# Kernel tuning notes

Hardware: AMD Instinct MI355X
Metric: run time of the kernel (lower is better)

The kernel has to match this reference:

```python
import jax, jax.numpy as jnp
import numpy as np

BEAM = 64  # min(beam_size=64, num_states=512)


def setup_inputs() -> dict:
    key = jax.random.key(0)
    ks = jax.random.split(key, 8)
    B, N, S, E, F, D = 8, 1024, 512, 2048, 256, 32
    unaries = jax.random.normal(ks[0], (B, N, S), jnp.float32)
    masks = jnp.ones((B, N), dtype=bool)
    binary_edges = jax.random.randint(ks[1], (B, E, 2), 0, N)
    binary_masks = jnp.ones((B, E), dtype=bool)
    node_features = jax.random.normal(ks[2], (B, N, F), jnp.float32)
    targets = jax.random.randint(ks[3], (B, N), 0, S)
    # learned params
    bin_embed = jax.random.uniform(ks[4], (2, S, D), jnp.float32)  # torch.rand init
    W_dyn = jax.random.normal(ks[5], (2 * F, D * D), jnp.float32) / jnp.sqrt(2.0 * F)
    b_dyn = jnp.zeros((D * D,), jnp.float32)
    return dict(unaries=unaries, masks=masks, binary_edges=binary_edges,
                binary_masks=binary_masks, node_features=node_features,
                targets=targets, bin_embed=bin_embed, W_dyn=W_dyn, b_dyn=b_dyn)


def reference(unaries, masks, binary_edges, binary_masks, node_features,
              targets, bin_embed, W_dyn, b_dyn):
    B, N, S = unaries.shape
    D = bin_embed.shape[-1]
    mf = masks.astype(unaries.dtype)
    un = unaries * mf[..., None]  # mask unaries

    # put target state first in the beam (scatter +inf, then topk indices)
    big = jnp.asarray(1e30, un.dtype)
    _un = jax.lax.stop_gradient(un).at[
        jnp.arange(B)[:, None], jnp.arange(N)[None, :], targets].set(big)
    _, beam_targets = jax.lax.top_k(_un, BEAM)               # [B,N,K] int
    beam_unary = jnp.take_along_axis(un, beam_targets, axis=2)  # [B,N,K]

    # gather beam state-ids and node features at edge endpoints
    e0, e1 = binary_edges[..., 0], binary_edges[..., 1]      # [B,E]
    bt0 = jnp.take_along_axis(beam_targets, e0[:, :, None], axis=1)  # [B,E,K]
    bt1 = jnp.take_along_axis(beam_targets, e1[:, :, None], axis=1)
    s0 = bin_embed[0][bt0]                                   # [B,E,K,D]
    s1 = bin_embed[1][bt1]                                   # [B,E,K,D]
    f0 = jnp.take_along_axis(node_features, e0[:, :, None], axis=1)  # [B,E,F]
    f1 = jnp.take_along_axis(node_features, e1[:, :, None], axis=1)
    feat = jnp.concatenate([f0, f1], axis=-1)                # [B,E,2F]
    ew = jax.nn.relu(feat @ W_dyn + b_dyn)                   # [B,E,D*D]
    ew = ew.reshape(B, -1, D, D)                             # [B,E,D,D]

    # low-rank binary potentials: B E K1 D1, B E D1 D2, B E K2 D2 -> B E K1 K2
    bin_phis = jnp.einsum('beki,beij,belj->bekl', s0, ew, s1)

    # piecewise pseudo-likelihood
    norm_unary = jax.nn.log_softmax(beam_unary, axis=-1)
    gold_unary = jnp.where(masks, norm_unary[:, :, 0], 0.0)
    pll = gold_unary.sum(-1)                                 # [B]

    E = bin_phis.shape[1]
    norm_bin = jax.nn.log_softmax(bin_phis.reshape(B, E, BEAM * BEAM), axis=-1)
    gold_bin = jnp.where(binary_masks, norm_bin[:, :, 0], 0.0)  # index (0,0)
    pll = pll + gold_bin.sum(-1)

    nll = -(pll / mf.sum(-1)).mean()
    return nll
```

## Files before the change

### kernel.cpp

```cpp
#include <hip/hip_runtime.h>
#include <hip/hip_bf16.h>
#include <math.h>

#define BATCH  8
#define NNODE  1024
#define NSTATE 512
#define NEDGE  2048
#define NFEAT  256
#define DDIM   32
#define KBEAM  64

typedef __attribute__((ext_vector_type(8))) short bf16x8;
typedef __attribute__((ext_vector_type(4))) float f32x4;
typedef unsigned short u16;
typedef unsigned long long u64;

__device__ __forceinline__ u16 f2b(float f) {
  __hip_bfloat16 h = __float2bfloat16(f);
  return *reinterpret_cast<u16*>(&h);
}

__global__ __launch_bounds__(256) void beam_kernel(
    const float* __restrict__ unaries,
    const int*   __restrict__ targets,
    int*         __restrict__ beam_ids,
    float*       __restrict__ ugold)
{
  const int tid  = threadIdx.x;
  const int lane = tid & 63, wid = tid >> 6;
  const int node = blockIdx.x * 4 + wid;
  const float* row = unaries + (size_t)node * NSTATE;
  const int target = targets[node];

  float v[8];
  float4 va = *(const float4*)(row + lane * 4);
  float4 vb = *(const float4*)(row + 256 + lane * 4);
  v[0]=va.x; v[1]=va.y; v[2]=va.z; v[3]=va.w;
  v[4]=vb.x; v[5]=vb.y; v[6]=vb.z; v[7]=vb.w;

  u64 key[8]; int idx[8];
  #pragma unroll
  for (int t = 0; t < 8; t++) {
    int i = (t < 4) ? lane * 4 + t : 256 + lane * 4 + (t - 4);
    idx[t] = i;
    unsigned u = __float_as_uint(v[t]);
    unsigned k = (u & 0x80000000u) ? ~u : (u | 0x80000000u);
    if (i == target) k = 0xFFFFFFFFu;
    key[t] = ((u64)k << 9) | (unsigned)(NSTATE - 1 - i);
  }

  unsigned act = 0xFFu;
  int K = KBEAM;
  for (int b = 40; b >= 0; b--) {
    unsigned m1 = 0;
    #pragma unroll
    for (int t = 0; t < 8; t++)
      m1 |= ((unsigned)((key[t] >> b) & 1ull)) << t;
    int c = __popc(m1 & act);
    #pragma unroll
    for (int off = 32; off > 0; off >>= 1) c += __shfl_xor(c, off);
    if (c >= K) act &= m1; else { K -= c; act = act & ~m1; }
  }
  u64 thr = 0;
  #pragma unroll
  for (int t = 0; t < 8; t++) if (act & (1u << t)) thr = key[t];
  {
    unsigned lo = (unsigned)thr, hi = (unsigned)(thr >> 32);
    #pragma unroll
    for (int off = 32; off > 0; off >>= 1) {
      lo |= __shfl_xor(lo, off); hi |= __shfl_xor(hi, off);
    }
    thr = ((u64)hi << 32) | lo;
  }

  unsigned sel = 0;
  #pragma unroll
  for (int t = 0; t < 8; t++) if (key[t] >= thr) sel |= 1u << t;

  float m = v[0];
  #pragma unroll
  for (int t = 1; t < 8; t++) m = fmaxf(m, v[t]);
  #pragma unroll
  for (int off = 32; off > 0; off >>= 1) m = fmaxf(m, __shfl_xor(m, off));
  float s = 0.0f, tv = 0.0f;
  #pragma unroll
  for (int t = 0; t < 8; t++) {
    if (sel & (1u << t)) s += __expf(v[t] - m);
    if (idx[t] == target) tv = v[t];
  }
  #pragma unroll
  for (int off = 32; off > 0; off >>= 1) {
    s += __shfl_xor(s, off); tv += __shfl_xor(tv, off);
  }
  if (lane == 0) ugold[node] = tv - (m + __logf(s));

  int* bout = beam_ids + (size_t)node * KBEAM;
  unsigned selnt = sel;
  #pragma unroll
  for (int t = 0; t < 8; t++)
    if (idx[t] == target) { selnt &= ~(1u << t); bout[0] = target; }
  int base = 1;
  #pragma unroll
  for (int t = 0; t < 8; t++) {
    u64 bt = __ballot((selnt >> t) & 1u);
    if ((selnt >> t) & 1u) {
      int pos = base + __popcll(bt & ((1ull << lane) - 1ull));
      bout[pos] = idx[t];
    }
    base += __popcll(bt);
  }
}

__global__ __launch_bounds__(256) void conv_embed_kernel(
    const float* __restrict__ in, u16* __restrict__ out) {
  int idx = (blockIdx.x * 256 + threadIdx.x) * 4;
  float4 v = *(const float4*)(in + idx);
  ushort4 o; o.x = f2b(v.x); o.y = f2b(v.y); o.z = f2b(v.z); o.w = f2b(v.w);
  *(ushort4*)(out + idx) = o;
}

__global__ __launch_bounds__(256) void convW_kernel(
    const float* __restrict__ W, u16* __restrict__ Wt) {
  __shared__ u16 tile[64][64];
  const int tid = threadIdx.x;
  const int n0 = blockIdx.x * 64;
  const int k0 = blockIdx.y * 64;
  #pragma unroll
  for (int p = 0; p < 4; p++) {
    int k  = (tid >> 4) + p * 16;
    int nc = (tid & 15) * 4;
    float4 v = *(const float4*)(W + (size_t)(k0 + k) * 1024 + n0 + nc);
    tile[nc + 0][k] = f2b(v.x); tile[nc + 1][k] = f2b(v.y);
    tile[nc + 2][k] = f2b(v.z); tile[nc + 3][k] = f2b(v.w);
  }
  __syncthreads();
  int n = tid >> 2, kc = (tid & 3) * 16;
  uint4 o0 = *(uint4*)&tile[n][kc];
  uint4 o1 = *(uint4*)&tile[n][kc + 8];
  *(uint4*)(Wt + (size_t)(n0 + n) * 512 + k0 + kc)     = o0;
  *(uint4*)(Wt + (size_t)(n0 + n) * 512 + k0 + kc + 8) = o1;
}

__global__ __launch_bounds__(128) void gatherA_kernel(
    const float* __restrict__ nf, const int* __restrict__ edges,
    u16* __restrict__ A) {
  const int eg = blockIdx.x;
  const int t  = threadIdx.x;
  const int b  = eg >> 11;
  const int n0 = edges[eg * 2 + 0], n1 = edges[eg * 2 + 1];
  const float* src = (t < 64)
      ? nf + ((size_t)(b * NNODE + n0) * NFEAT) + t * 4
      : nf + ((size_t)(b * NNODE + n1) * NFEAT) + (t - 64) * 4;
  float4 v = *(const float4*)src;
  ushort4 o; o.x = f2b(v.x); o.y = f2b(v.y); o.z = f2b(v.z); o.w = f2b(v.w);
  *(ushort4*)(A + (size_t)eg * 512 + t * 4) = o;
}

__global__ __launch_bounds__(256) void gemm_mfma_kernel(
    const u16* __restrict__ A,
    const u16* __restrict__ Bt,
    const float* __restrict__ bias,
    u16* __restrict__ ew)
{
  __shared__ u16 As[128 * 32];
  __shared__ u16 Bs[128 * 32];
  const int tid  = threadIdx.x;
  const int lane = tid & 63, wid = tid >> 6;
  const int wr = wid >> 1, wc = wid & 1;
  const int fr = lane & 15, fg = lane >> 4;
  const int row0 = blockIdx.y * 128, col0 = blockIdx.x * 128;

  const int sr = tid >> 2, sc = (tid & 3) * 8;
  const u16* aptr  = A  + (size_t)(row0 + sr) * 512 + sc;
  const u16* bptr  = Bt + (size_t)(col0 + sr) * 512 + sc;
  const u16* aptr2 = aptr + (size_t)64 * 512;
  const u16* bptr2 = bptr + (size_t)64 * 512;

  f32x4 acc[4][4] = {};
  uint4 ra  = *(const uint4*)aptr,  ra2 = *(const uint4*)aptr2;
  uint4 rb  = *(const uint4*)bptr,  rb2 = *(const uint4*)bptr2;

  for (int ks = 0; ks < 16; ks++) {
    __syncthreads();
    *(uint4*)&As[sr * 32 + sc]        = ra;
    *(uint4*)&As[(sr + 64) * 32 + sc] = ra2;
    *(uint4*)&Bs[sr * 32 + sc]        = rb;
    *(uint4*)&Bs[(sr + 64) * 32 + sc] = rb2;
    __syncthreads();
    if (ks < 15) {
      int ko = (ks + 1) * 32;
      ra  = *(const uint4*)(aptr  + ko); ra2 = *(const uint4*)(aptr2 + ko);
      rb  = *(const uint4*)(bptr  + ko); rb2 = *(const uint4*)(bptr2 + ko);
    }
    bf16x8 af[4], bfr[4];
    #pragma unroll
    for (int mb = 0; mb < 4; mb++)
      af[mb] = *(bf16x8*)&As[(wr * 64 + mb * 16 + fr) * 32 + fg * 8];
    #pragma unroll
    for (int nb = 0; nb < 4; nb++)
      bfr[nb] = *(bf16x8*)&Bs[(wc * 64 + nb * 16 + fr) * 32 + fg * 8];
    #pragma unroll
    for (int mb = 0; mb < 4; mb++)
      #pragma unroll
      for (int nb = 0; nb < 4; nb++)
        acc[mb][nb] = __builtin_amdgcn_mfma_f32_16x16x32_bf16(
            af[mb], bfr[nb], acc[mb][nb], 0, 0, 0);
  }

  #pragma unroll
  for (int nb = 0; nb < 4; nb++) {
    int col = col0 + wc * 64 + nb * 16 + fr;
    float bc = bias[col];
    #pragma unroll
    for (int mb = 0; mb < 4; mb++) {
      #pragma unroll
      for (int r = 0; r < 4; r++) {
        int rowm = row0 + wr * 64 + mb * 16 + fg * 4 + r;
        float v = fmaxf(acc[mb][nb][r] + bc, 0.0f);
        ew[(size_t)rowm * 1024 + col] = f2b(v);
      }
    }
  }
}

#define EW_LDS 5120
__global__ __launch_bounds__(256) void edge_mfma_kernel(
    const u16* __restrict__ embed,
    const int* __restrict__ edges,
    const u16* __restrict__ ewb,
    const int* __restrict__ beam_ids,
    float*     __restrict__ egold)
{
  __shared__ u16 esh[4 * EW_LDS];
  const int tid  = threadIdx.x;
  const int lane = tid & 63, wid = tid >> 6;
  u16* s0  = &esh[wid * EW_LDS];
  u16* s1u = s0 + 2048;
  u16* ewl = s0 + 4096;

  const int eg = blockIdx.x * 4 + wid;
  const int b  = eg >> 11;
  const int n0 = edges[eg * 2 + 0], n1 = edges[eg * 2 + 1];
  const int bt0 = beam_ids[(size_t)(b * NNODE + n0) * KBEAM + lane];
  const int bt1 = beam_ids[(size_t)(b * NNODE + n1) * KBEAM + lane];

  #pragma unroll
  for (int s = 0; s < 4; s++) {
    int r = s * 16 + (lane >> 2);
    int e0 = __shfl(bt0, r), e1 = __shfl(bt1, r);
    uint4 v0 = *(const uint4*)(embed + (size_t)e0 * DDIM + (lane & 3) * 8);
    uint4 v1 = *(const uint4*)(embed + (size_t)NSTATE * DDIM
                               + (size_t)e1 * DDIM + (lane & 3) * 8);
    *(uint4*)&s0 [r * 32 + (lane & 3) * 8] = v0;
    *(uint4*)&s1u[r * 32 + (lane & 3) * 8] = v1;
  }
  #pragma unroll
  for (int s = 0; s < 2; s++) {
    uint4 v = *(const uint4*)(ewb + (size_t)eg * 1024 + s * 512 + lane * 8);
    *(uint4*)&ewl[s * 512 + lane * 8] = v;
  }
  asm volatile("s_waitcnt lgkmcnt(0)" ::: "memory");

  const int fr = lane & 15, fg = lane >> 4;
  bf16x8 a1[4], bew[2];
  #pragma unroll
  for (int mb = 0; mb < 4; mb++)
    a1[mb] = *(bf16x8*)&s1u[(mb * 16 + fr) * 32 + fg * 8];
  #pragma unroll
  for (int nb = 0; nb < 2; nb++)
    bew[nb] = *(bf16x8*)&ewl[(nb * 16 + fr) * 32 + fg * 8];
  f32x4 uacc[4][2] = {};
  #pragma unroll
  for (int mb = 0; mb < 4; mb++)
    #pragma unroll
    for (int nb = 0; nb < 2; nb++)
      uacc[mb][nb] = __builtin_amdgcn_mfma_f32_16x16x32_bf16(
          a1[mb], bew[nb], uacc[mb][nb], 0, 0, 0);

  asm volatile("s_waitcnt lgkmcnt(0)" ::: "memory");
  #pragma unroll
  for (int mb = 0; mb < 4; mb++)
    #pragma unroll
    for (int nb = 0; nb < 2; nb++)
      #pragma unroll
      for (int r = 0; r < 4; r++) {
        int l = mb * 16 + fg * 4 + r;
        int i = nb * 16 + fr;
        s1u[l * 32 + i] = f2b(uacc[mb][nb][r]);
      }
  asm volatile("s_waitcnt lgkmcnt(0)" ::: "memory");

  bf16x8 a0[4], bu[4];
  #pragma unroll
  for (int mb = 0; mb < 4; mb++)
    a0[mb] = *(bf16x8*)&s0[(mb * 16 + fr) * 32 + fg * 8];
  #pragma unroll
  for (int nb = 0; nb < 4; nb++)
    bu[nb] = *(bf16x8*)&s1u[(nb * 16 + fr) * 32 + fg * 8];
  f32x4 facc[4][4] = {};
  #pragma unroll
  for (int mb = 0; mb < 4; mb++)
    #pragma unroll
    for (int nb = 0; nb < 4; nb++)
      facc[mb][nb] = __builtin_amdgcn_mfma_f32_16x16x32_bf16(
          a0[mb], bu[nb], facc[mb][nb], 0, 0, 0);

  float mx = -INFINITY;
  #pragma unroll
  for (int mb = 0; mb < 4; mb++)
    #pragma unroll
    for (int nb = 0; nb < 4; nb++)
      #pragma unroll
      for (int r = 0; r < 4; r++) mx = fmaxf(mx, facc[mb][nb][r]);
  #pragma unroll
  for (int off = 32; off > 0; off >>= 1) mx = fmaxf(mx, __shfl_xor(mx, off));
  float s = 0.0f;
  #pragma unroll
  for (int mb = 0; mb < 4; mb++)
    #pragma unroll
    for (int nb = 0; nb < 4; nb++)
      #pragma unroll
      for (int r = 0; r < 4; r++) s += __expf(facc[mb][nb][r] - mx);
  #pragma unroll
  for (int off = 32; off > 0; off >>= 1) s += __shfl_xor(s, off);
  if (lane == 0) {
    egold[eg] = facc[0][0][0] - mx - __logf(s);
  }
}

__global__ __launch_bounds__(1024) void reduce_kernel(
    const float* __restrict__ ugold,
    const float* __restrict__ egold,
    float* __restrict__ out) {
  __shared__ float red[16];
  const int tid = threadIdx.x;
  float s = 0.0f;
  #pragma unroll
  for (int t = 0; t < 8; t++)  s += ugold[tid + t * 1024];
  #pragma unroll
  for (int t = 0; t < 16; t++) s += egold[tid + t * 1024];
  #pragma unroll
  for (int off = 32; off > 0; off >>= 1) s += __shfl_xor(s, off);
  if ((tid & 63) == 0) red[tid >> 6] = s;
  __syncthreads();
  if (tid == 0) {
    float tot = 0.0f;
    #pragma unroll
    for (int w = 0; w < 16; w++) tot += red[w];
    out[0] = -tot / (float)(BATCH * NNODE);
  }
}

extern "C" void kernel_launch(void* const* d_in, const int* in_sizes, int n_in,
                              void* d_out, int out_size, void* d_ws, size_t ws_size,
                              hipStream_t stream) {
  (void)in_sizes; (void)n_in; (void)out_size; (void)ws_size;
  const float* unaries   = (const float*)d_in[0];
  const int*   edges     = (const int*)  d_in[2];
  const float* nf        = (const float*)d_in[4];
  const int*   targets   = (const int*)  d_in[5];
  const float* bin_embed = (const float*)d_in[6];
  const float* W         = (const float*)d_in[7];
  const float* bias      = (const float*)d_in[8];
  float* out = (float*)d_out;

  char* ws = (char*)d_ws;
  float* ugold = (float*)ws;
  float* egold = (float*)(ws + (32u<<10));
  int*  beam_ids = (int*)(ws + (1u<<20));
  u16*  Abf = (u16*)(ws + (3u<<20));
  u16*  Wt  = (u16*)(ws + (19u<<20));
  u16*  ewb = (u16*)(ws + (20u<<20));
  u16*  emb = (u16*)(ws + (52u<<20));

  beam_kernel<<<BATCH * NNODE / 4, 256, 0, stream>>>(unaries, targets, beam_ids, ugold);
  conv_embed_kernel<<<32, 256, 0, stream>>>(bin_embed, emb);
  convW_kernel<<<dim3(16, 8), 256, 0, stream>>>(W, Wt);
  gatherA_kernel<<<BATCH * NEDGE, 128, 0, stream>>>(nf, edges, Abf);
  gemm_mfma_kernel<<<dim3(8, 128), 256, 0, stream>>>(Abf, Wt, bias, ewb);
  edge_mfma_kernel<<<BATCH * NEDGE / 4, 256, 0, stream>>>(emb, edges, ewb, beam_ids, egold);
  reduce_kernel<<<1, 1024, 0, stream>>>(ugold, egold, out);
}
```

Measured before the change: 182.0 us.

## Use ballot-based radix select, direct LDS loads in GEMM, and fewer kernels

The beam top-k radix select now counts with ballots instead of shuffle reductions, broadcasts the threshold with a single shuffle, and fetches the target value from its owning lane. Two conversion kernels are merged into one launch. The GEMM stages tiles with global_load_lds straight into LDS, dropping the register prefetch, which loses the overlap of the next tile's load with the current MFMAs. The edge kernel loads MFMA operands directly from global memory instead of staging them through LDS, which cuts LDS traffic and footprint but relies on caches for the gathered embedding rows.

```diff
diff --git a/kernel.cpp b/kernel.cpp
--- a/kernel.cpp
+++ b/kernel.cpp
@@ -56,22 +56,19 @@
     #pragma unroll
     for (int t = 0; t < 8; t++)
       m1 |= ((unsigned)((key[t] >> b) & 1ull)) << t;
-    int c = __popc(m1 & act);
-    #pragma unroll
-    for (int off = 32; off > 0; off >>= 1) c += __shfl_xor(c, off);
-    if (c >= K) act &= m1; else { K -= c; act = act & ~m1; }
-  }
+    unsigned ma = m1 & act;
+    int c = 0;
+    #pragma unroll
+    for (int t = 0; t < 8; t++)
+      c += __popcll(__ballot((ma >> t) & 1u));
+    if (c >= K) act = ma; else { K -= c; act &= ~m1; }
+  }
+  u64 lm = __ballot(act != 0);
+  int srclane = __ffsll((long long)lm) - 1;
   u64 thr = 0;
   #pragma unroll
-  for (int t = 0; t < 8; t++) if (act & (1u << t)) thr = key[t];
-  {
-    unsigned lo = (unsigned)thr, hi = (unsigned)(thr >> 32);
-    #pragma unroll
-    for (int off = 32; off > 0; off >>= 1) {
-      lo |= __shfl_xor(lo, off); hi |= __shfl_xor(hi, off);
-    }
-    thr = ((u64)hi << 32) | lo;
-  }
+  for (int t = 0; t < 8; t++) if ((act >> t) & 1u) thr = key[t];
+  thr = __shfl(thr, srclane);
 
   unsigned sel = 0;
   #pragma unroll
@@ -82,16 +79,20 @@
   for (int t = 1; t < 8; t++) m = fmaxf(m, v[t]);
   #pragma unroll
   for (int off = 32; off > 0; off >>= 1) m = fmaxf(m, __shfl_xor(m, off));
-  float s = 0.0f, tv = 0.0f;
-  #pragma unroll
-  for (int t = 0; t < 8; t++) {
+  float s = 0.0f;
+  #pragma unroll
+  for (int t = 0; t < 8; t++)
     if (sel & (1u << t)) s += __expf(v[t] - m);
-    if (idx[t] == target) tv = v[t];
-  }
-  #pragma unroll
-  for (int off = 32; off > 0; off >>= 1) {
-    s += __shfl_xor(s, off); tv += __shfl_xor(tv, off);
-  }
+  #pragma unroll
+  for (int off = 32; off > 0; off >>= 1) s += __shfl_xor(s, off);
+
+  int tl, ts;
+  if (target < 256) { tl = target >> 2; ts = target & 3; }
+  else { tl = (target - 256) >> 2; ts = 4 + ((target - 256) & 3); }
+  float tvl = 0.0f;
+  #pragma unroll
+  for (int t = 0; t < 8; t++) if (t == ts) tvl = v[t];
+  float tv = __shfl(tvl, tl);
   if (lane == 0) ugold[node] = tv - (m + __logf(s));
 
   int* bout = beam_ids + (size_t)node * KBEAM;
@@ -111,20 +112,20 @@
   }
 }
 
-__global__ __launch_bounds__(256) void conv_embed_kernel(
-    const float* __restrict__ in, u16* __restrict__ out) {
-  int idx = (blockIdx.x * 256 + threadIdx.x) * 4;
-  float4 v = *(const float4*)(in + idx);
-  ushort4 o; o.x = f2b(v.x); o.y = f2b(v.y); o.z = f2b(v.z); o.w = f2b(v.w);
-  *(ushort4*)(out + idx) = o;
-}
-
-__global__ __launch_bounds__(256) void convW_kernel(
-    const float* __restrict__ W, u16* __restrict__ Wt) {
+__global__ __launch_bounds__(256) void conv_kernel(
+    const float* __restrict__ W, u16* __restrict__ Wt,
+    const float* __restrict__ bin_embed, u16* __restrict__ emb) {
   __shared__ u16 tile[64][64];
   const int tid = threadIdx.x;
-  const int n0 = blockIdx.x * 64;
-  const int k0 = blockIdx.y * 64;
+  if (blockIdx.x >= 128) {
+    int idx = ((blockIdx.x - 128) * 256 + tid) * 4;
+    float4 v = *(const float4*)(bin_embed + idx);
+    ushort4 o; o.x = f2b(v.x); o.y = f2b(v.y); o.z = f2b(v.z); o.w = f2b(v.w);
+    *(ushort4*)(emb + idx) = o;
+    return;
+  }
+  const int n0 = (blockIdx.x & 15) * 64;
+  const int k0 = (blockIdx.x >> 4) * 64;
   #pragma unroll
   for (int p = 0; p < 4; p++) {
     int k  = (tid >> 4) + p * 16;
@@ -170,28 +171,36 @@
   const int fr = lane & 15, fg = lane >> 4;
   const int row0 = blockIdx.y * 128, col0 = blockIdx.x * 128;
 
-  const int sr = tid >> 2, sc = (tid & 3) * 8;
-  const u16* aptr  = A  + (size_t)(row0 + sr) * 512 + sc;
-  const u16* bptr  = Bt + (size_t)(col0 + sr) * 512 + sc;
-  const u16* aptr2 = aptr + (size_t)64 * 512;
-  const u16* bptr2 = bptr + (size_t)64 * 512;
+  const int r0 = wid * 32;
+  const int rs = r0 + (lane >> 2);
+  const int cs = (lane & 3) * 8;
+  const u16* ga0 = A  + (size_t)(row0 + rs) * 512 + cs;
+  const u16* ga1 = ga0 + (size_t)16 * 512;
+  const u16* gb0 = Bt + (size_t)(col0 + rs) * 512 + cs;
+  const u16* gb1 = gb0 + (size_t)16 * 512;
+  u16* la0 = &As[r0 * 32];
+  u16* la1 = &As[(r0 + 16) * 32];
+  u16* lb0 = &Bs[r0 * 32];
+  u16* lb1 = &Bs[(r0 + 16) * 32];
 
   f32x4 acc[4][4] = {};
-  uint4 ra  = *(const uint4*)aptr,  ra2 = *(const uint4*)aptr2;
-  uint4 rb  = *(const uint4*)bptr,  rb2 = *(const uint4*)bptr2;
-
   for (int ks = 0; ks < 16; ks++) {
+    const int ko = ks * 32;
     __syncthreads();
-    *(uint4*)&As[sr * 32 + sc]        = ra;
-    *(uint4*)&As[(sr + 64) * 32 + sc] = ra2;
-    *(uint4*)&Bs[sr * 32 + sc]        = rb;
-    *(uint4*)&Bs[(sr + 64) * 32 + sc] = rb2;
+    __builtin_amdgcn_global_load_lds(
+        (const __attribute__((address_space(1))) unsigned int*)(ga0 + ko),
+        (__attribute__((address_space(3))) unsigned int*)la0, 16, 0, 0);
+    __builtin_amdgcn_global_load_lds(
+        (const __attribute__((address_space(1))) unsigned int*)(ga1 + ko),
+        (__attribute__((address_space(3))) unsigned int*)la1, 16, 0, 0);
+    __builtin_amdgcn_global_load_lds(
+        (const __attribute__((address_space(1))) unsigned int*)(gb0 + ko),
+        (__attribute__((address_space(3))) unsigned int*)lb0, 16, 0, 0);
+    __builtin_amdgcn_global_load_lds(
+        (const __attribute__((address_space(1))) unsigned int*)(gb1 + ko),
+        (__attribute__((address_space(3))) unsigned int*)lb1, 16, 0, 0);
     __syncthreads();
-    if (ks < 15) {
-      int ko = (ks + 1) * 32;
-      ra  = *(const uint4*)(aptr  + ko); ra2 = *(const uint4*)(aptr2 + ko);
-      rb  = *(const uint4*)(bptr  + ko); rb2 = *(const uint4*)(bptr2 + ko);
-    }
+
     bf16x8 af[4], bfr[4];
     #pragma unroll
     for (int mb = 0; mb < 4; mb++)
@@ -223,7 +232,6 @@
   }
 }
 
-#define EW_LDS 5120
 __global__ __launch_bounds__(256) void edge_mfma_kernel(
     const u16* __restrict__ embed,
     const int* __restrict__ edges,
@@ -231,44 +239,27 @@
     const int* __restrict__ beam_ids,
     float*     __restrict__ egold)
 {
-  __shared__ u16 esh[4 * EW_LDS];
+  __shared__ u16 ush[4 * 2048];
   const int tid  = threadIdx.x;
   const int lane = tid & 63, wid = tid >> 6;
-  u16* s0  = &esh[wid * EW_LDS];
-  u16* s1u = s0 + 2048;
-  u16* ewl = s0 + 4096;
+  u16* ul = &ush[wid * 2048];
 
   const int eg = blockIdx.x * 4 + wid;
   const int b  = eg >> 11;
   const int n0 = edges[eg * 2 + 0], n1 = edges[eg * 2 + 1];
   const int bt0 = beam_ids[(size_t)(b * NNODE + n0) * KBEAM + lane];
   const int bt1 = beam_ids[(size_t)(b * NNODE + n1) * KBEAM + lane];
-
-  #pragma unroll
-  for (int s = 0; s < 4; s++) {
-    int r = s * 16 + (lane >> 2);
-    int e0 = __shfl(bt0, r), e1 = __shfl(bt1, r);
-    uint4 v0 = *(const uint4*)(embed + (size_t)e0 * DDIM + (lane & 3) * 8);
-    uint4 v1 = *(const uint4*)(embed + (size_t)NSTATE * DDIM
-                               + (size_t)e1 * DDIM + (lane & 3) * 8);
-    *(uint4*)&s0 [r * 32 + (lane & 3) * 8] = v0;
-    *(uint4*)&s1u[r * 32 + (lane & 3) * 8] = v1;
-  }
-  #pragma unroll
-  for (int s = 0; s < 2; s++) {
-    uint4 v = *(const uint4*)(ewb + (size_t)eg * 1024 + s * 512 + lane * 8);
-    *(uint4*)&ewl[s * 512 + lane * 8] = v;
-  }
-  asm volatile("s_waitcnt lgkmcnt(0)" ::: "memory");
-
   const int fr = lane & 15, fg = lane >> 4;
+
   bf16x8 a1[4], bew[2];
   #pragma unroll
-  for (int mb = 0; mb < 4; mb++)
-    a1[mb] = *(bf16x8*)&s1u[(mb * 16 + fr) * 32 + fg * 8];
+  for (int mb = 0; mb < 4; mb++) {
+    int r = __shfl(bt1, mb * 16 + fr);
+    a1[mb] = *(const bf16x8*)(embed + (size_t)NSTATE * DDIM + (size_t)r * DDIM + fg * 8);
+  }
   #pragma unroll
   for (int nb = 0; nb < 2; nb++)
-    bew[nb] = *(bf16x8*)&ewl[(nb * 16 + fr) * 32 + fg * 8];
+    bew[nb] = *(const bf16x8*)(ewb + (size_t)eg * 1024 + (nb * 16 + fr) * 32 + fg * 8);
   f32x4 uacc[4][2] = {};
   #pragma unroll
   for (int mb = 0; mb < 4; mb++)
@@ -277,26 +268,25 @@
       uacc[mb][nb] = __builtin_amdgcn_mfma_f32_16x16x32_bf16(
           a1[mb], bew[nb], uacc[mb][nb], 0, 0, 0);
 
+  #pragma unroll
+  for (int mb = 0; mb < 4; mb++)
+    #pragma unroll
+    for (int nb = 0; nb < 2; nb++)
+      #pragma unroll
+      for (int r = 0; r < 4; r++)
+        ul[(mb * 16 + fg * 4 + r) * 32 + nb * 16 + fr] = f2b(uacc[mb][nb][r]);
   asm volatile("s_waitcnt lgkmcnt(0)" ::: "memory");
-  #pragma unroll
-  for (int mb = 0; mb < 4; mb++)
-    #pragma unroll
-    for (int nb = 0; nb < 2; nb++)
-      #pragma unroll
-      for (int r = 0; r < 4; r++) {
-        int l = mb * 16 + fg * 4 + r;
-        int i = nb * 16 + fr;
-        s1u[l * 32 + i] = f2b(uacc[mb][nb][r]);
-      }
-  asm volatile("s_waitcnt lgkmcnt(0)" ::: "memory");
+  __builtin_amdgcn_sched_barrier(0);
 
   bf16x8 a0[4], bu[4];
   #pragma unroll
-  for (int mb = 0; mb < 4; mb++)
-    a0[mb] = *(bf16x8*)&s0[(mb * 16 + fr) * 32 + fg * 8];
+  for (int mb = 0; mb < 4; mb++) {
+    int r = __shfl(bt0, mb * 16 + fr);
+    a0[mb] = *(const bf16x8*)(embed + (size_t)r * DDIM + fg * 8);
+  }
   #pragma unroll
   for (int nb = 0; nb < 4; nb++)
-    bu[nb] = *(bf16x8*)&s1u[(nb * 16 + fr) * 32 + fg * 8];
+    bu[nb] = *(bf16x8*)&ul[(nb * 16 + fr) * 32 + fg * 8];
   f32x4 facc[4][4] = {};
   #pragma unroll
   for (int mb = 0; mb < 4; mb++)
@@ -374,8 +364,7 @@
   u16*  emb = (u16*)(ws + (52u<<20));
 
   beam_kernel<<<BATCH * NNODE / 4, 256, 0, stream>>>(unaries, targets, beam_ids, ugold);
-  conv_embed_kernel<<<32, 256, 0, stream>>>(bin_embed, emb);
-  convW_kernel<<<dim3(16, 8), 256, 0, stream>>>(W, Wt);
+  conv_kernel<<<160, 256, 0, stream>>>(W, Wt, bin_embed, emb);
   gatherA_kernel<<<BATCH * NEDGE, 128, 0, stream>>>(nf, edges, Abf);
   gemm_mfma_kernel<<<dim3(8, 128), 256, 0, stream>>>(Abf, Wt, bias, ewb);
   edge_mfma_kernel<<<BATCH * NEDGE / 4, 256, 0, stream>>>(emb, edges, ewb, beam_ids, egold);
```

Measured after the change: 182.9 us. Within noise of the previous version (+0.5%).
